# Performance work log

Measured on AMD Instinct MI355X. Metric: run time of the kernel, lower is better.

## Reference

```python
import jax, jax.numpy as jnp
import numpy as np

N_NODES = 50000
N_EDGES = 800000


def _sage_mean(x, src, dst, w, W_self, W_neigh, b, n_nodes):
    # DGL SAGEConv('mean') with edge_weight: messages m_e = w_e * h[src_e],
    # h_neigh[v] = sum_{e->v} m_e / in_degree(v)  (zero if no in-edges),
    # out = h @ W_self + h_neigh @ W_neigh + b
    msg = x[src] * w[:, None]                                   # [E, d]
    s = jax.ops.segment_sum(msg, dst, num_segments=n_nodes)     # [N, d]
    deg = jax.ops.segment_sum(jnp.ones_like(w), dst, num_segments=n_nodes)
    h_neigh = s / jnp.clip(deg, 1.0)[:, None]
    return x @ W_self + h_neigh @ W_neigh + b


def setup_inputs() -> dict:
    key = jax.random.key(0)
    ks = jax.random.split(key, 12)
    d_in, d_h = 64, 256
    inp = {
        'features': jax.random.normal(ks[0], (N_NODES, d_in), dtype=jnp.float32),
        'edge_src': jax.random.randint(ks[1], (N_EDGES,), 0, N_NODES, dtype=jnp.int32),
        'edge_dst': jax.random.randint(ks[2], (N_EDGES,), 0, N_NODES, dtype=jnp.int32),
        'edge_weights': jax.random.uniform(ks[3], (N_EDGES,), dtype=jnp.float32),
        'W1_self': jax.random.normal(ks[4], (d_in, d_h), dtype=jnp.float32) * (1.0 / np.sqrt(d_in)),
        'W1_neigh': jax.random.normal(ks[5], (d_in, d_h), dtype=jnp.float32) * (1.0 / np.sqrt(d_in)),
        'b1': jnp.zeros((d_h,), dtype=jnp.float32),
        'W2_self': jax.random.normal(ks[6], (d_h, 128), dtype=jnp.float32) * (1.0 / np.sqrt(d_h)),
        'W2_neigh': jax.random.normal(ks[7], (d_h, 128), dtype=jnp.float32) * (1.0 / np.sqrt(d_h)),
        'b2': jnp.zeros((128,), dtype=jnp.float32),
        'Wl1': jax.random.normal(ks[8], (128, 64), dtype=jnp.float32) * (1.0 / np.sqrt(128)),
        'bl1': jnp.zeros((64,), dtype=jnp.float32),
        'Wl2': jax.random.normal(ks[9], (64, 32), dtype=jnp.float32) * (1.0 / np.sqrt(64)),
        'bl2': jnp.zeros((32,), dtype=jnp.float32),
        'Wl3': jax.random.normal(ks[10], (32, 10), dtype=jnp.float32) * (1.0 / np.sqrt(32)),
        'bl3': jnp.zeros((10,), dtype=jnp.float32),
    }
    return inp


def reference(features, edge_src, edge_dst, edge_weights,
              W1_self, W1_neigh, b1, W2_self, W2_neigh, b2,
              Wl1, bl1, Wl2, bl2, Wl3, bl3):
    n = features.shape[0]
    x = features.reshape(n, -1)  # flatten (already 2D)
    x = jax.nn.relu(_sage_mean(x, edge_src, edge_dst, edge_weights,
                               W1_self, W1_neigh, b1, n))
    # conv2 is applied twice on identical inputs in the original; results are equal
    embeddings = _sage_mean(x, edge_src, edge_dst, edge_weights,
                            W2_self, W2_neigh, b2, n)
    h = jax.nn.relu(embeddings @ Wl1 + bl1)
    h = jax.nn.relu(h @ Wl2 + bl2)
    out = h @ Wl3 + bl3
    return (out, embeddings)
```

## Files before the change

### kernel.cpp

```cpp
#include <hip/hip_runtime.h>
#include <hip/hip_bf16.h>

#define N_NODES 50000
#define N_EDGES 800000
#define MT_TILES 3125

#define NBLK_SORT 200
#define CHUNK_SORT 4000
#define NBKT 196

typedef __attribute__((ext_vector_type(8))) short frag_ab;
typedef __attribute__((ext_vector_type(4))) float frag_cd;

static __device__ __forceinline__ unsigned short f2b(float f) {
    union { float f; unsigned u; } v; v.f = f;
    unsigned r = v.u + 0x7fffu + ((v.u >> 16) & 1u);
    return (unsigned short)(r >> 16);
}
static __device__ __forceinline__ float b2f(unsigned short b) {
    union { float f; unsigned u; } v; v.u = ((unsigned)b) << 16;
    return v.f;
}
static __device__ __forceinline__ float blo(unsigned p) { return b2f((unsigned short)(p & 0xffffu)); }
static __device__ __forceinline__ float bhi(unsigned p) { return b2f((unsigned short)(p >> 16)); }

static __device__ __forceinline__ unsigned short packBK_elem(const float* __restrict__ Wa,
                                                             const float* __restrict__ Wb,
                                                             int Ka, int N, int idx) {
    int j = idx & 7;
    int lane = (idx >> 3) & 63;
    int rest = idx >> 9;
    int ntiles = N >> 4;
    int nt = rest % ntiles;
    int kt = rest / ntiles;
    int kk = kt * 32 + (lane >> 4) * 8 + j;
    int nn = nt * 16 + (lane & 15);
    float v = (kk < Ka) ? Wa[kk * N + nn] : Wb[(kk - Ka) * N + nn];
    return f2b(v);
}
static __device__ __forceinline__ unsigned short packBN_elem(const float* __restrict__ Wa,
                                                             const float* __restrict__ Wb,
                                                             int Na, int N, int idx) {
    int j = idx & 7;
    int lane = (idx >> 3) & 63;
    int rest = idx >> 9;
    int ntiles = N >> 4;
    int nt = rest % ntiles;
    int kt = rest / ntiles;
    int kk = kt * 32 + (lane >> 4) * 8 + j;
    int nn = nt * 16 + (lane & 15);
    float v = (nn < Na) ? Wa[kk * Na + nn] : Wb[kk * (N - Na) + (nn - Na)];
    return f2b(v);
}

#define PREP_S0 800000
#define PREP_S1 (PREP_S0 + 32768)
#define PREP_S2 (PREP_S1 + 65536)
#define PREP_S3 (PREP_S2 + 8192)
#define PREP_S4 (PREP_S3 + 2048)
#define PREP_BLKS 3549

__global__ __launch_bounds__(256) void prep_p1_kernel(const float4* __restrict__ x4,
                                                      ushort4* __restrict__ xb4,
                                                      const float* __restrict__ W1s,
                                                      const float* __restrict__ W1n,
                                                      const float* __restrict__ W2s,
                                                      const float* __restrict__ W2n,
                                                      const float* __restrict__ Wl1,
                                                      const float* __restrict__ Wl2,
                                                      unsigned short* __restrict__ B1p,
                                                      unsigned short* __restrict__ B2p,
                                                      unsigned short* __restrict__ Bl1p,
                                                      unsigned short* __restrict__ Bl2p,
                                                      const int* __restrict__ dst,
                                                      int* __restrict__ G) {
    __shared__ int h[256];
    int bid = blockIdx.x;
    int t = threadIdx.x;
    if (bid >= PREP_BLKS) {
        int blk = bid - PREP_BLKS;
        h[t] = 0;
        __syncthreads();
        int base = blk * CHUNK_SORT;
        for (int i = t; i < CHUNK_SORT; i += 256)
            atomicAdd(&h[dst[base + i] >> 8], 1);
        __syncthreads();
        G[blk * 256 + t] = h[t];
        return;
    }
    int idx = bid * 256 + t;
    if (idx < PREP_S0) {
        float4 v = x4[idx];
        ushort4 o;
        o.x = f2b(v.x); o.y = f2b(v.y); o.z = f2b(v.z); o.w = f2b(v.w);
        xb4[idx] = o;
    } else if (idx < PREP_S1) {
        int i = idx - PREP_S0;
        B1p[i] = packBK_elem(W1s, W1n, 64, 256, i);
    } else if (idx < PREP_S2) {
        int i = idx - PREP_S1;
        B2p[i] = packBN_elem(W2s, W2n, 128, 256, i);
    } else if (idx < PREP_S3) {
        int i = idx - PREP_S2;
        Bl1p[i] = packBK_elem(Wl1, Wl1, 128, 64, i);
    } else {
        int i = idx - PREP_S3;
        Bl2p[i] = packBK_elem(Wl2, Wl2, 64, 32, i);
    }
}


__global__ __launch_bounds__(256) void p2a_scan(int* __restrict__ G,
                                                int* __restrict__ colsum) {
    __shared__ int sc[256];
    int b = blockIdx.x;
    int t = threadIdx.x;
    int v = (t < NBLK_SORT) ? G[t * 256 + b] : 0;
    sc[t] = v;
    __syncthreads();
    for (int off = 1; off < 256; off <<= 1) {
        int add = (t >= off) ? sc[t - off] : 0;
        __syncthreads();
        sc[t] += add;
        __syncthreads();
    }
    if (t < NBLK_SORT) G[t * 256 + b] = sc[t] - v;
    if (t == 255) colsum[b] = sc[255];
}

__global__ __launch_bounds__(256) void p3_scatter(const int* __restrict__ src,
                                                  const int* __restrict__ dst,
                                                  const float* __restrict__ w,
                                                  const int* __restrict__ G,
                                                  const int* __restrict__ colsum,
                                                  int* __restrict__ bdst,
                                                  int2* __restrict__ bsedge) {
    __shared__ int cur[256];
    __shared__ int sc[256];
    int t = threadIdx.x;
    int v = colsum[t];
    sc[t] = v;
    __syncthreads();
    for (int off = 1; off < 256; off <<= 1) {
        int add = (t >= off) ? sc[t - off] : 0;
        __syncthreads();
        sc[t] += add;
        __syncthreads();
    }
    cur[t] = G[blockIdx.x * 256 + t] + (sc[t] - v);
    __syncthreads();
    int base = blockIdx.x * CHUNK_SORT;
    for (int i = t; i < CHUNK_SORT; i += 256) {
        int e = base + i;
        int d = dst[e];
        int pos = atomicAdd(&cur[d >> 8], 1);
        bdst[pos] = d;
        bsedge[pos] = make_int2(src[e], __float_as_int(w[e]));
    }
}

__global__ __launch_bounds__(256) void p4_sort(const int* __restrict__ colsum,
                                               const int* __restrict__ bdst,
                                               const int2* __restrict__ bsedge,
                                               int* __restrict__ row_off,
                                               float* __restrict__ inv_deg,
                                               int2* __restrict__ sedge) {
    __shared__ int lcnt[256];
    __shared__ int lcur[256];
    __shared__ int sc[256];
    __shared__ int sE0, sE1;
    int t = threadIdx.x;
    int b = blockIdx.x;
    int cv = colsum[t];
    sc[t] = cv;
    __syncthreads();
    for (int off = 1; off < 256; off <<= 1) {
        int add = (t >= off) ? sc[t - off] : 0;
        __syncthreads();
        sc[t] += add;
        __syncthreads();
    }
    if (t == b) { sE0 = sc[t] - cv; sE1 = sc[t]; }
    lcnt[t] = 0;
    __syncthreads();
    int e0 = sE0, e1 = sE1;
    int d0 = b << 8;
    for (int e = e0 + t; e < e1; e += 256)
        atomicAdd(&lcnt[bdst[e] - d0], 1);
    __syncthreads();
    int v = lcnt[t];
    sc[t] = v;
    __syncthreads();
    for (int off = 1; off < 256; off <<= 1) {
        int add = (t >= off) ? sc[t - off] : 0;
        __syncthreads();
        sc[t] += add;
        __syncthreads();
    }
    int loff = e0 + sc[t] - v;
    lcur[t] = loff;
    int d = d0 + t;
    if (d < N_NODES) {
        row_off[d] = loff;
        inv_deg[d] = 1.0f / (float)(v > 0 ? v : 1);
    }
    if (b == 0 && t == 0) row_off[N_NODES] = N_EDGES;
    __syncthreads();
    for (int e = e0 + t; e < e1; e += 256) {
        int dd = bdst[e];
        int2 sv = bsedge[e];
        int pos = atomicAdd(&lcur[dd - d0], 1);
        sedge[pos] = sv;
    }
}


__global__ __launch_bounds__(256) void agg64_kernel(const uint4* __restrict__ xb4,
                                                    const int* __restrict__ row_off,
                                                    const int2* __restrict__ sedge,
                                                    const float* __restrict__ inv_deg,
                                                    uint4* __restrict__ hn1b4) {
    int tid = threadIdx.x;
    int lane = tid & 63;
    int er = lane >> 3;
    int l7 = lane & 7;
    int n = blockIdx.x * 4 + (tid >> 6);
    if (n >= N_NODES) return;
    int e0 = row_off[n], e1 = row_off[n + 1];
    float id = inv_deg[n];
    float a[8];
    #pragma unroll
    for (int j = 0; j < 8; j++) a[j] = 0.f;
    int e1m1 = e1 - 1;
    for (int e = e0; e < e1; e += 16) {
        int2 m[2];
        uint4 p[2];
        float w[2];
        #pragma unroll
        for (int k = 0; k < 2; k++) {
            int ee = e + k * 8 + er;
            int idx = ee < e1 ? ee : e1m1;
            m[k] = sedge[idx];
        }
        #pragma unroll
        for (int k = 0; k < 2; k++) {
            p[k] = xb4[m[k].x * 8 + l7];
            int ee = e + k * 8 + er;
            w[k] = (ee < e1) ? __int_as_float(m[k].y) : 0.f;
        }
        #pragma unroll
        for (int k = 0; k < 2; k++) {
            a[0] += w[k] * blo(p[k].x); a[1] += w[k] * bhi(p[k].x);
            a[2] += w[k] * blo(p[k].y); a[3] += w[k] * bhi(p[k].y);
            a[4] += w[k] * blo(p[k].z); a[5] += w[k] * bhi(p[k].z);
            a[6] += w[k] * blo(p[k].w); a[7] += w[k] * bhi(p[k].w);
        }
    }
    #pragma unroll
    for (int j = 0; j < 8; j++) {
        a[j] += __shfl_xor(a[j], 8, 64);
        a[j] += __shfl_xor(a[j], 16, 64);
        a[j] += __shfl_xor(a[j], 32, 64);
    }
    if (er == 0) {
        uint4 o;
        o.x = (unsigned)f2b(a[0] * id) | ((unsigned)f2b(a[1] * id) << 16);
        o.y = (unsigned)f2b(a[2] * id) | ((unsigned)f2b(a[3] * id) << 16);
        o.z = (unsigned)f2b(a[4] * id) | ((unsigned)f2b(a[5] * id) << 16);
        o.w = (unsigned)f2b(a[6] * id) | ((unsigned)f2b(a[7] * id) << 16);
        hn1b4[n * 8 + l7] = o;
    }
}

__global__ __launch_bounds__(256) void agg128_kernel(const uint4* __restrict__ zb4,
                                                     const int* __restrict__ row_off,
                                                     const int2* __restrict__ sedge,
                                                     const float* __restrict__ inv_deg,
                                                     float* __restrict__ emb,
                                                     uint4* __restrict__ embb4) {
    int tid = threadIdx.x;
    int lane = tid & 63;
    int qr = lane >> 4;
    int l15 = lane & 15;
    int n = blockIdx.x * 4 + (tid >> 6);
    if (n >= N_NODES) return;
    int e0 = row_off[n], e1 = row_off[n + 1];
    float id = inv_deg[n];
    float4 s0, s1;
    if (qr == 0) {
        s0 = ((const float4*)emb)[n * 32 + l15 * 2];
        s1 = ((const float4*)emb)[n * 32 + l15 * 2 + 1];
    }
    float a[8];
    #pragma unroll
    for (int j = 0; j < 8; j++) a[j] = 0.f;
    int e1m1 = e1 - 1;
    for (int e = e0; e < e1; e += 16) {
        int2 m[4];
        uint4 p[4];
        float w[4];
        #pragma unroll
        for (int k = 0; k < 4; k++) {
            int ee = e + k * 4 + qr;
            int idx = ee < e1 ? ee : e1m1;
            m[k] = sedge[idx];
        }
        #pragma unroll
        for (int k = 0; k < 4; k++) {
            p[k] = zb4[m[k].x * 16 + l15];
            int ee = e + k * 4 + qr;
            w[k] = (ee < e1) ? __int_as_float(m[k].y) : 0.f;
        }
        #pragma unroll
        for (int k = 0; k < 4; k++) {
            a[0] += w[k] * blo(p[k].x); a[1] += w[k] * bhi(p[k].x);
            a[2] += w[k] * blo(p[k].y); a[3] += w[k] * bhi(p[k].y);
            a[4] += w[k] * blo(p[k].z); a[5] += w[k] * bhi(p[k].z);
            a[6] += w[k] * blo(p[k].w); a[7] += w[k] * bhi(p[k].w);
        }
    }
    #pragma unroll
    for (int j = 0; j < 8; j++) {
        a[j] += __shfl_xor(a[j], 16, 64);
        a[j] += __shfl_xor(a[j], 32, 64);
    }
    if (qr == 0) {
        float v0 = s0.x + a[0] * id;
        float v1 = s0.y + a[1] * id;
        float v2 = s0.z + a[2] * id;
        float v3 = s0.w + a[3] * id;
        float v4 = s1.x + a[4] * id;
        float v5 = s1.y + a[5] * id;
        float v6 = s1.z + a[6] * id;
        float v7 = s1.w + a[7] * id;
        ((float4*)emb)[n * 32 + l15 * 2]     = make_float4(v0, v1, v2, v3);
        ((float4*)emb)[n * 32 + l15 * 2 + 1] = make_float4(v4, v5, v6, v7);
        uint4 o;
        o.x = (unsigned)f2b(v0) | ((unsigned)f2b(v1) << 16);
        o.y = (unsigned)f2b(v2) | ((unsigned)f2b(v3) << 16);
        o.z = (unsigned)f2b(v4) | ((unsigned)f2b(v5) << 16);
        o.w = (unsigned)f2b(v6) | ((unsigned)f2b(v7) << 16);
        embb4[n * 16 + l15] = o;
    }
}


__global__ __launch_bounds__(512) void gemm1_mfma(const unsigned short* __restrict__ xb,
                                                  const unsigned short* __restrict__ hn1b,
                                                  const unsigned short* __restrict__ Bp,
                                                  const float* __restrict__ b1,
                                                  unsigned short* __restrict__ x1b) {
    __shared__ __align__(16) unsigned short sB[2][8192];
    int tid = threadIdx.x;
    int lane = tid & 63;
    int wv = tid >> 6;
    int mt = blockIdx.x * 8 + wv;
    if (mt >= MT_TILES) mt = MT_TILES - 1;
    int q = lane >> 4;
    int rl = lane & 15;
    int row = mt * 16 + rl;
    frag_ab a[4];
    a[0] = *(const frag_ab*)(xb + row * 64 + q * 8);
    a[1] = *(const frag_ab*)(xb + row * 64 + q * 8 + 32);
    a[2] = *(const frag_ab*)(hn1b + row * 64 + q * 8);
    a[3] = *(const frag_ab*)(hn1b + row * 64 + q * 8 + 32);
    frag_cd acc[16];
    #pragma unroll
    for (int nt = 0; nt < 16; nt++) acc[nt] = (frag_cd){0.f, 0.f, 0.f, 0.f};
    const float4* gB = (const float4*)Bp;
    float4 s0 = gB[tid], s1 = gB[512 + tid];
    ((float4*)sB[0])[tid] = s0;
    ((float4*)sB[0])[512 + tid] = s1;
    #pragma unroll
    for (int kt = 0; kt < 4; kt++) {
        __syncthreads();
        if (kt < 3) { s0 = gB[(kt + 1) * 1024 + tid]; s1 = gB[(kt + 1) * 1024 + 512 + tid]; }
        const unsigned short* sb = sB[kt & 1];
        #pragma unroll
        for (int nt = 0; nt < 16; nt++) {
            frag_ab b = *(const frag_ab*)(sb + (nt * 64 + lane) * 8);
            acc[nt] = __builtin_amdgcn_mfma_f32_16x16x32_bf16(a[kt], b, acc[nt], 0, 0, 0);
        }
        if (kt < 3) {
            ((float4*)sB[(kt + 1) & 1])[tid] = s0;
            ((float4*)sB[(kt + 1) & 1])[512 + tid] = s1;
        }
    }
    int r0 = mt * 16;
    #pragma unroll
    for (int nt = 0; nt < 16; nt++) {
        int c = nt * 16 + rl;
        float bias = b1[c];
        #pragma unroll
        for (int i = 0; i < 4; i++) {
            int r = r0 + q * 4 + i;
            float v = acc[nt][i] + bias;
            v = v > 0.f ? v : 0.f;
            x1b[r * 256 + c] = f2b(v);
        }
    }
}

__global__ __launch_bounds__(512) void gemm2_mfma(const unsigned short* __restrict__ x1b,
                                                  const unsigned short* __restrict__ Bp,
                                                  const float* __restrict__ b2,
                                                  float* __restrict__ emb,
                                                  unsigned short* __restrict__ zb) {
    __shared__ __align__(16) unsigned short sB[2][8192];
    int tid = threadIdx.x;
    int lane = tid & 63;
    int wv = tid >> 6;
    int mt = blockIdx.x * 8 + wv;
    if (mt >= MT_TILES) mt = MT_TILES - 1;
    int q = lane >> 4;
    int rl = lane & 15;
    int row = mt * 16 + rl;
    const unsigned short* arow = x1b + row * 256 + q * 8;
    frag_ab a[8];
    #pragma unroll
    for (int kt = 0; kt < 8; kt++) a[kt] = *(const frag_ab*)(arow + kt * 32);
    frag_cd acc[16];
    #pragma unroll
    for (int nt = 0; nt < 16; nt++) acc[nt] = (frag_cd){0.f, 0.f, 0.f, 0.f};
    const float4* gB = (const float4*)Bp;
    float4 s0 = gB[tid], s1 = gB[512 + tid];
    ((float4*)sB[0])[tid] = s0;
    ((float4*)sB[0])[512 + tid] = s1;
    #pragma unroll
    for (int kt = 0; kt < 8; kt++) {
        __syncthreads();
        if (kt < 7) { s0 = gB[(kt + 1) * 1024 + tid]; s1 = gB[(kt + 1) * 1024 + 512 + tid]; }
        const unsigned short* sb = sB[kt & 1];
        #pragma unroll
        for (int nt = 0; nt < 16; nt++) {
            frag_ab b = *(const frag_ab*)(sb + (nt * 64 + lane) * 8);
            acc[nt] = __builtin_amdgcn_mfma_f32_16x16x32_bf16(a[kt], b, acc[nt], 0, 0, 0);
        }
        if (kt < 7) {
            ((float4*)sB[(kt + 1) & 1])[tid] = s0;
            ((float4*)sB[(kt + 1) & 1])[512 + tid] = s1;
        }
    }
    int r0 = mt * 16;
    #pragma unroll
    for (int nt = 0; nt < 8; nt++) {
        int c = nt * 16 + rl;
        float bias = b2[c];
        #pragma unroll
        for (int i = 0; i < 4; i++) {
            int r = r0 + q * 4 + i;
            emb[r * 128 + c] = acc[nt][i] + bias;
        }
    }
    #pragma unroll
    for (int nt = 8; nt < 16; nt++) {
        int c = (nt - 8) * 16 + rl;
        #pragma unroll
        for (int i = 0; i < 4; i++) {
            int r = r0 + q * 4 + i;
            zb[r * 128 + c] = f2b(acc[nt][i]);
        }
    }
}

__global__ __launch_bounds__(256) void mlp_fused(const unsigned short* __restrict__ embb,
                                                 const unsigned short* __restrict__ B1,
                                                 const float* __restrict__ bl1,
                                                 const unsigned short* __restrict__ B2,
                                                 const float* __restrict__ bl2,
                                                 const float* __restrict__ Wl3,
                                                 const float* __restrict__ bl3,
                                                 float* __restrict__ out) {
    __shared__ __align__(16) unsigned short h64s[64 * 72];
    __shared__ float hs[64][33];
    int tid = threadIdx.x;
    int lane = tid & 63;
    int wv = tid >> 6;
    int mt = blockIdx.x * 4 + wv;
    if (mt >= MT_TILES) mt = MT_TILES - 1;
    int q = lane >> 4;
    int rl = lane & 15;
    const unsigned short* arow = embb + (mt * 16 + rl) * 128 + q * 8;
    const frag_ab* bp1 = (const frag_ab*)B1;
    frag_cd acc[4];
    #pragma unroll
    for (int nt = 0; nt < 4; nt++) acc[nt] = (frag_cd){0.f, 0.f, 0.f, 0.f};
    #pragma unroll
    for (int kt = 0; kt < 4; kt++) {
        frag_ab a = *(const frag_ab*)(arow + kt * 32);
        #pragma unroll
        for (int nt = 0; nt < 4; nt++)
            acc[nt] = __builtin_amdgcn_mfma_f32_16x16x32_bf16(a, bp1[(kt * 4 + nt) * 64 + lane], acc[nt], 0, 0, 0);
    }
    #pragma unroll
    for (int nt = 0; nt < 4; nt++) {
        int c = nt * 16 + rl;
        float bias = bl1[c];
        #pragma unroll
        for (int i = 0; i < 4; i++) {
            float v = acc[nt][i] + bias;
            h64s[(wv * 16 + q * 4 + i) * 72 + c] = f2b(v > 0.f ? v : 0.f);
        }
    }
    __syncthreads();
    const unsigned short* a2 = h64s + (wv * 16 + rl) * 72 + q * 8;
    const frag_ab* bp2 = (const frag_ab*)B2;
    frag_cd acc2[2];
    #pragma unroll
    for (int nt = 0; nt < 2; nt++) acc2[nt] = (frag_cd){0.f, 0.f, 0.f, 0.f};
    #pragma unroll
    for (int kt = 0; kt < 2; kt++) {
        frag_ab a = *(const frag_ab*)(a2 + kt * 32);
        #pragma unroll
        for (int nt = 0; nt < 2; nt++)
            acc2[nt] = __builtin_amdgcn_mfma_f32_16x16x32_bf16(a, bp2[(kt * 2 + nt) * 64 + lane], acc2[nt], 0, 0, 0);
    }
    #pragma unroll
    for (int nt = 0; nt < 2; nt++) {
        int c = nt * 16 + rl;
        float bias = bl2[c];
        #pragma unroll
        for (int i = 0; i < 4; i++) {
            int lr = wv * 16 + q * 4 + i;
            float v = acc2[nt][i] + bias;
            hs[lr][c] = v > 0.f ? v : 0.f;
        }
    }
    __syncthreads();
    int base = blockIdx.x * 64;
    for (int idx = tid; idx < 640; idx += 256) {
        int lr = idx / 10;
        int j = idx - lr * 10;
        int n = base + lr;
        if (n < N_NODES) {
            float a = bl3[j];
            #pragma unroll
            for (int k = 0; k < 32; k++) a += hs[lr][k] * Wl3[k * 10 + j];
            out[n * 10 + j] = a;
        }
    }
}


extern "C" void kernel_launch(void* const* d_in, const int* in_sizes, int n_in,
                              void* d_out, int out_size, void* d_ws, size_t ws_size,
                              hipStream_t stream) {
    const float* x   = (const float*)d_in[0];
    const int* esrc  = (const int*)d_in[1];
    const int* edst  = (const int*)d_in[2];
    const float* ew  = (const float*)d_in[3];
    const float* W1s = (const float*)d_in[4];
    const float* W1n = (const float*)d_in[5];
    const float* b1  = (const float*)d_in[6];
    const float* W2s = (const float*)d_in[7];
    const float* W2n = (const float*)d_in[8];
    const float* b2  = (const float*)d_in[9];
    const float* Wl1 = (const float*)d_in[10];
    const float* bl1 = (const float*)d_in[11];
    const float* Wl2 = (const float*)d_in[12];
    const float* bl2 = (const float*)d_in[13];
    const float* Wl3 = (const float*)d_in[14];
    const float* bl3 = (const float*)d_in[15];

    float* out = (float*)d_out;
    float* emb = out + 500000;

    char* ws = (char*)d_ws;
    size_t off = 0;
    auto alloc = [&](size_t bytes) -> void* {
        void* p = ws + off;
        off = (off + bytes + 255) & ~(size_t)255;
        return p;
    };
    int*   row_off = (int*)alloc((size_t)(N_NODES + 1) * 4);
    float* inv_deg = (float*)alloc((size_t)N_NODES * 4);
    int*   G       = (int*)alloc((size_t)NBLK_SORT * 256 * 4);
    int*   colsum  = (int*)alloc(256 * 4);
    int*   bdst    = (int*)alloc((size_t)N_EDGES * 4);
    int2*  bsedge  = (int2*)alloc((size_t)N_EDGES * 8);
    int2*  sedge   = (int2*)alloc((size_t)N_EDGES * 8);
    unsigned short* xb   = (unsigned short*)alloc((size_t)N_NODES * 64 * 2);
    unsigned short* hn1b = (unsigned short*)alloc((size_t)N_NODES * 64 * 2);
    unsigned short* x1b  = (unsigned short*)alloc((size_t)N_NODES * 256 * 2);
    unsigned short* zb   = (unsigned short*)alloc((size_t)N_NODES * 128 * 2);
    unsigned short* embb = (unsigned short*)alloc((size_t)N_NODES * 128 * 2);
    unsigned short* B1p  = (unsigned short*)alloc(128 * 256 * 2);
    unsigned short* B2p  = (unsigned short*)alloc(256 * 256 * 2);
    unsigned short* Bl1p = (unsigned short*)alloc(128 * 64 * 2);
    unsigned short* Bl2p = (unsigned short*)alloc(64 * 32 * 2);

    prep_p1_kernel<<<PREP_BLKS + NBLK_SORT, 256, 0, stream>>>(
        (const float4*)x, (ushort4*)xb, W1s, W1n, W2s, W2n, Wl1, Wl2,
        B1p, B2p, Bl1p, Bl2p, edst, G);

    p2a_scan<<<256, 256, 0, stream>>>(G, colsum);
    p3_scatter<<<NBLK_SORT, 256, 0, stream>>>(esrc, edst, ew, G, colsum, bdst, bsedge);
    p4_sort<<<NBKT, 256, 0, stream>>>(colsum, bdst, bsedge, row_off, inv_deg, sedge);

    const int GBLK8 = (MT_TILES + 7) / 8;
    const int GBLK  = (MT_TILES + 3) / 4;
    const int ABLK  = (N_NODES + 3) / 4;

    agg64_kernel<<<ABLK, 256, 0, stream>>>((const uint4*)xb, row_off, sedge,
                                           inv_deg, (uint4*)hn1b);
    gemm1_mfma<<<GBLK8, 512, 0, stream>>>(xb, hn1b, B1p, b1, x1b);

    gemm2_mfma<<<GBLK8, 512, 0, stream>>>(x1b, B2p, b2, emb, zb);
    agg128_kernel<<<ABLK, 256, 0, stream>>>((const uint4*)zb, row_off, sedge,
                                            inv_deg, emb, (uint4*)embb);

    mlp_fused<<<GBLK, 256, 0, stream>>>(embb, Bl1p, bl1, Bl2p, bl2, Wl3, bl3, out);
}
```

Before: 234.1 us.

## Fuse layer-1 and layer-2 GEMMs via LDS, drop bf16 embedding copy, widen sort

Merges gemm1 and gemm2 into one kernel that keeps the ReLU'd 256-wide hidden tile in shared memory instead of writing x1b to global memory and reading it back. The agg128 kernel no longer writes a bf16 copy of the embeddings; mlp_fused instead reads fp32 emb and converts it to bf16 in registers. The sort now uses 400 blocks of 2000 edges, and the scan handles two block entries per thread. The fused GEMM drops to 256-thread blocks with a single-buffered B tile and two barriers per k-step, which may lower overlap and occupancy because of the large LDS footprint.

```diff
diff --git a/kernel.cpp b/kernel.cpp
--- a/kernel.cpp
+++ b/kernel.cpp
@@ -5,8 +5,8 @@
 #define N_EDGES 800000
 #define MT_TILES 3125
 
-#define NBLK_SORT 200
-#define CHUNK_SORT 4000
+#define NBLK_SORT 400
+#define CHUNK_SORT 2000
 #define NBKT 196
 
 typedef __attribute__((ext_vector_type(8))) short frag_ab;
@@ -115,7 +115,10 @@
     __shared__ int sc[256];
     int b = blockIdx.x;
     int t = threadIdx.x;
-    int v = (t < NBLK_SORT) ? G[t * 256 + b] : 0;
+    int j0 = 2 * t, j1 = 2 * t + 1;
+    int v0 = (j0 < NBLK_SORT) ? G[j0 * 256 + b] : 0;
+    int v1 = (j1 < NBLK_SORT) ? G[j1 * 256 + b] : 0;
+    int v = v0 + v1;
     sc[t] = v;
     __syncthreads();
     for (int off = 1; off < 256; off <<= 1) {
@@ -124,7 +127,9 @@
         sc[t] += add;
         __syncthreads();
     }
-    if (t < NBLK_SORT) G[t * 256 + b] = sc[t] - v;
+    int ex = sc[t] - v;
+    if (j0 < NBLK_SORT) G[j0 * 256 + b] = ex;
+    if (j1 < NBLK_SORT) G[j1 * 256 + b] = ex + v0;
     if (t == 255) colsum[b] = sc[255];
 }
 
@@ -276,8 +281,7 @@
                                                      const int* __restrict__ row_off,
                                                      const int2* __restrict__ sedge,
                                                      const float* __restrict__ inv_deg,
-                                                     float* __restrict__ emb,
-                                                     uint4* __restrict__ embb4) {
+                                                     float* __restrict__ emb) {
     int tid = threadIdx.x;
     int lane = tid & 63;
     int qr = lane >> 4;
@@ -335,26 +339,23 @@
         float v7 = s1.w + a[7] * id;
         ((float4*)emb)[n * 32 + l15 * 2]     = make_float4(v0, v1, v2, v3);
         ((float4*)emb)[n * 32 + l15 * 2 + 1] = make_float4(v4, v5, v6, v7);
-        uint4 o;
-        o.x = (unsigned)f2b(v0) | ((unsigned)f2b(v1) << 16);
-        o.y = (unsigned)f2b(v2) | ((unsigned)f2b(v3) << 16);
-        o.z = (unsigned)f2b(v4) | ((unsigned)f2b(v5) << 16);
-        o.w = (unsigned)f2b(v6) | ((unsigned)f2b(v7) << 16);
-        embb4[n * 16 + l15] = o;
-    }
-}
-
-
-__global__ __launch_bounds__(512) void gemm1_mfma(const unsigned short* __restrict__ xb,
-                                                  const unsigned short* __restrict__ hn1b,
-                                                  const unsigned short* __restrict__ Bp,
-                                                  const float* __restrict__ b1,
-                                                  unsigned short* __restrict__ x1b) {
-    __shared__ __align__(16) unsigned short sB[2][8192];
+    }
+}
+
+__global__ __launch_bounds__(256) void gemm12_mfma(const unsigned short* __restrict__ xb,
+                                                   const unsigned short* __restrict__ hn1b,
+                                                   const unsigned short* __restrict__ B1p,
+                                                   const float* __restrict__ b1,
+                                                   const unsigned short* __restrict__ B2p,
+                                                   const float* __restrict__ b2,
+                                                   float* __restrict__ emb,
+                                                   unsigned short* __restrict__ zb) {
+    __shared__ __align__(16) unsigned short xS[64 * 264];
+    __shared__ __align__(16) unsigned short sB[8192];
     int tid = threadIdx.x;
     int lane = tid & 63;
     int wv = tid >> 6;
-    int mt = blockIdx.x * 8 + wv;
+    int mt = blockIdx.x * 4 + wv;
     if (mt >= MT_TILES) mt = MT_TILES - 1;
     int q = lane >> 4;
     int rl = lane & 15;
@@ -367,78 +368,60 @@
     frag_cd acc[16];
     #pragma unroll
     for (int nt = 0; nt < 16; nt++) acc[nt] = (frag_cd){0.f, 0.f, 0.f, 0.f};
-    const float4* gB = (const float4*)Bp;
-    float4 s0 = gB[tid], s1 = gB[512 + tid];
-    ((float4*)sB[0])[tid] = s0;
-    ((float4*)sB[0])[512 + tid] = s1;
+    const float4* gB = (const float4*)B1p;
+    float4 s0 = gB[tid], s1 = gB[256 + tid], s2 = gB[512 + tid], s3 = gB[768 + tid];
     #pragma unroll
     for (int kt = 0; kt < 4; kt++) {
         __syncthreads();
-        if (kt < 3) { s0 = gB[(kt + 1) * 1024 + tid]; s1 = gB[(kt + 1) * 1024 + 512 + tid]; }
-        const unsigned short* sb = sB[kt & 1];
+        ((float4*)sB)[tid] = s0;
+        ((float4*)sB)[256 + tid] = s1;
+        ((float4*)sB)[512 + tid] = s2;
+        ((float4*)sB)[768 + tid] = s3;
+        __syncthreads();
+        if (kt < 3) {
+            s0 = gB[(kt + 1) * 1024 + tid];       s1 = gB[(kt + 1) * 1024 + 256 + tid];
+            s2 = gB[(kt + 1) * 1024 + 512 + tid]; s3 = gB[(kt + 1) * 1024 + 768 + tid];
+        }
         #pragma unroll
         for (int nt = 0; nt < 16; nt++) {
-            frag_ab b = *(const frag_ab*)(sb + (nt * 64 + lane) * 8);
+            frag_ab b = *(const frag_ab*)(sB + (nt * 64 + lane) * 8);
             acc[nt] = __builtin_amdgcn_mfma_f32_16x16x32_bf16(a[kt], b, acc[nt], 0, 0, 0);
         }
-        if (kt < 3) {
-            ((float4*)sB[(kt + 1) & 1])[tid] = s0;
-            ((float4*)sB[(kt + 1) & 1])[512 + tid] = s1;
-        }
-    }
-    int r0 = mt * 16;
+    }
     #pragma unroll
     for (int nt = 0; nt < 16; nt++) {
         int c = nt * 16 + rl;
         float bias = b1[c];
         #pragma unroll
         for (int i = 0; i < 4; i++) {
-            int r = r0 + q * 4 + i;
             float v = acc[nt][i] + bias;
             v = v > 0.f ? v : 0.f;
-            x1b[r * 256 + c] = f2b(v);
-        }
-    }
-}
-
-__global__ __launch_bounds__(512) void gemm2_mfma(const unsigned short* __restrict__ x1b,
-                                                  const unsigned short* __restrict__ Bp,
-                                                  const float* __restrict__ b2,
-                                                  float* __restrict__ emb,
-                                                  unsigned short* __restrict__ zb) {
-    __shared__ __align__(16) unsigned short sB[2][8192];
-    int tid = threadIdx.x;
-    int lane = tid & 63;
-    int wv = tid >> 6;
-    int mt = blockIdx.x * 8 + wv;
-    if (mt >= MT_TILES) mt = MT_TILES - 1;
-    int q = lane >> 4;
-    int rl = lane & 15;
-    int row = mt * 16 + rl;
-    const unsigned short* arow = x1b + row * 256 + q * 8;
-    frag_ab a[8];
-    #pragma unroll
-    for (int kt = 0; kt < 8; kt++) a[kt] = *(const frag_ab*)(arow + kt * 32);
-    frag_cd acc[16];
-    #pragma unroll
-    for (int nt = 0; nt < 16; nt++) acc[nt] = (frag_cd){0.f, 0.f, 0.f, 0.f};
-    const float4* gB = (const float4*)Bp;
-    float4 s0 = gB[tid], s1 = gB[512 + tid];
-    ((float4*)sB[0])[tid] = s0;
-    ((float4*)sB[0])[512 + tid] = s1;
+            xS[(wv * 16 + q * 4 + i) * 264 + c] = f2b(v);
+        }
+    }
+    const float4* gB2 = (const float4*)B2p;
+    s0 = gB2[tid]; s1 = gB2[256 + tid]; s2 = gB2[512 + tid]; s3 = gB2[768 + tid];
+    frag_cd acc2[16];
+    #pragma unroll
+    for (int nt = 0; nt < 16; nt++) acc2[nt] = (frag_cd){0.f, 0.f, 0.f, 0.f};
+    const unsigned short* a2base = xS + (wv * 16 + rl) * 264 + q * 8;
     #pragma unroll
     for (int kt = 0; kt < 8; kt++) {
         __syncthreads();
-        if (kt < 7) { s0 = gB[(kt + 1) * 1024 + tid]; s1 = gB[(kt + 1) * 1024 + 512 + tid]; }
-        const unsigned short* sb = sB[kt & 1];
+        ((float4*)sB)[tid] = s0;
+        ((float4*)sB)[256 + tid] = s1;
+        ((float4*)sB)[512 + tid] = s2;
+        ((float4*)sB)[768 + tid] = s3;
+        __syncthreads();
+        if (kt < 7) {
+            s0 = gB2[(kt + 1) * 1024 + tid];       s1 = gB2[(kt + 1) * 1024 + 256 + tid];
+            s2 = gB2[(kt + 1) * 1024 + 512 + tid]; s3 = gB2[(kt + 1) * 1024 + 768 + tid];
+        }
+        frag_ab a2 = *(const frag_ab*)(a2base + kt * 32);
         #pragma unroll
         for (int nt = 0; nt < 16; nt++) {
-            frag_ab b = *(const frag_ab*)(sb + (nt * 64 + lane) * 8);
-            acc[nt] = __builtin_amdgcn_mfma_f32_16x16x32_bf16(a[kt], b, acc[nt], 0, 0, 0);
-        }
-        if (kt < 7) {
-            ((float4*)sB[(kt + 1) & 1])[tid] = s0;
-            ((float4*)sB[(kt + 1) & 1])[512 + tid] = s1;
+            frag_ab b = *(const frag_ab*)(sB + (nt * 64 + lane) * 8);
+            acc2[nt] = __builtin_amdgcn_mfma_f32_16x16x32_bf16(a2, b, acc2[nt], 0, 0, 0);
         }
     }
     int r0 = mt * 16;
@@ -449,7 +432,7 @@
         #pragma unroll
         for (int i = 0; i < 4; i++) {
             int r = r0 + q * 4 + i;
-            emb[r * 128 + c] = acc[nt][i] + bias;
+            emb[r * 128 + c] = acc2[nt][i] + bias;
         }
     }
     #pragma unroll
@@ -458,12 +441,12 @@
         #pragma unroll
         for (int i = 0; i < 4; i++) {
             int r = r0 + q * 4 + i;
-            zb[r * 128 + c] = f2b(acc[nt][i]);
-        }
-    }
-}
-
-__global__ __launch_bounds__(256) void mlp_fused(const unsigned short* __restrict__ embb,
+            zb[r * 128 + c] = f2b(acc2[nt][i]);
+        }
+    }
+}
+
+__global__ __launch_bounds__(256) void mlp_fused(const float* __restrict__ emb,
                                                  const unsigned short* __restrict__ B1,
                                                  const float* __restrict__ bl1,
                                                  const unsigned short* __restrict__ B2,
@@ -480,14 +463,19 @@
     if (mt >= MT_TILES) mt = MT_TILES - 1;
     int q = lane >> 4;
     int rl = lane & 15;
-    const unsigned short* arow = embb + (mt * 16 + rl) * 128 + q * 8;
     const frag_ab* bp1 = (const frag_ab*)B1;
     frag_cd acc[4];
     #pragma unroll
     for (int nt = 0; nt < 4; nt++) acc[nt] = (frag_cd){0.f, 0.f, 0.f, 0.f};
     #pragma unroll
     for (int kt = 0; kt < 4; kt++) {
-        frag_ab a = *(const frag_ab*)(arow + kt * 32);
+        const float4* ap = (const float4*)(emb + (mt * 16 + rl) * 128 + kt * 32 + q * 8);
+        float4 f0 = ap[0], f1 = ap[1];
+        frag_ab a;
+        a[0] = (short)f2b(f0.x); a[1] = (short)f2b(f0.y);
+        a[2] = (short)f2b(f0.z); a[3] = (short)f2b(f0.w);
+        a[4] = (short)f2b(f1.x); a[5] = (short)f2b(f1.y);
+        a[6] = (short)f2b(f1.z); a[7] = (short)f2b(f1.w);
         #pragma unroll
         for (int nt = 0; nt < 4; nt++)
             acc[nt] = __builtin_amdgcn_mfma_f32_16x16x32_bf16(a, bp1[(kt * 4 + nt) * 64 + lane], acc[nt], 0, 0, 0);
@@ -581,9 +569,7 @@
     int2*  sedge   = (int2*)alloc((size_t)N_EDGES * 8);
     unsigned short* xb   = (unsigned short*)alloc((size_t)N_NODES * 64 * 2);
     unsigned short* hn1b = (unsigned short*)alloc((size_t)N_NODES * 64 * 2);
-    unsigned short* x1b  = (unsigned short*)alloc((size_t)N_NODES * 256 * 2);
     unsigned short* zb   = (unsigned short*)alloc((size_t)N_NODES * 128 * 2);
-    unsigned short* embb = (unsigned short*)alloc((size_t)N_NODES * 128 * 2);
     unsigned short* B1p  = (unsigned short*)alloc(128 * 256 * 2);
     unsigned short* B2p  = (unsigned short*)alloc(256 * 256 * 2);
     unsigned short* Bl1p = (unsigned short*)alloc(128 * 64 * 2);
@@ -597,17 +583,15 @@
     p3_scatter<<<NBLK_SORT, 256, 0, stream>>>(esrc, edst, ew, G, colsum, bdst, bsedge);
     p4_sort<<<NBKT, 256, 0, stream>>>(colsum, bdst, bsedge, row_off, inv_deg, sedge);
 
-    const int GBLK8 = (MT_TILES + 7) / 8;
-    const int GBLK  = (MT_TILES + 3) / 4;
-    const int ABLK  = (N_NODES + 3) / 4;
+    const int GBLK = (MT_TILES + 3) / 4;
+    const int ABLK = (N_NODES + 3) / 4;
 
     agg64_kernel<<<ABLK, 256, 0, stream>>>((const uint4*)xb, row_off, sedge,
                                            inv_deg, (uint4*)hn1b);
-    gemm1_mfma<<<GBLK8, 512, 0, stream>>>(xb, hn1b, B1p, b1, x1b);
-
-    gemm2_mfma<<<GBLK8, 512, 0, stream>>>(x1b, B2p, b2, emb, zb);
+    gemm12_mfma<<<GBLK, 256, 0, stream>>>(xb, hn1b, B1p, b1, B2p, b2, emb, zb);
+
     agg128_kernel<<<ABLK, 256, 0, stream>>>((const uint4*)zb, row_off, sedge,
-                                            inv_deg, emb, (uint4*)embb);
-
-    mlp_fused<<<GBLK, 256, 0, stream>>>(embb, Bl1p, bl1, Bl2p, bl2, Wl3, bl3, out);
-}
+                                            inv_deg, emb);
+
+    mlp_fused<<<GBLK, 256, 0, stream>>>(emb, Bl1p, bl1, Bl2p, bl2, Wl3, bl3, out);
+}
```

Result: slower. 241.7 us (+3.2%).

## Drop bf16 embedding copy, convert fp32 embeddings in MLP; double sort blocks

Applied to the files above, without the earlier changes.

agg128 no longer writes a bf16 copy of the embeddings. mlp_fused now reads the fp32 embeddings directly and converts them to bf16 in registers before the MFMA. This saves one 12.8MB write but doubles the read traffic of the MLP input. Separately, the edge-sort partition now uses 400 blocks of 2000 edges instead of 200 of 4000, and the scan handles two block rows per thread.

```diff
diff --git a/kernel.cpp b/kernel.cpp
--- a/kernel.cpp
+++ b/kernel.cpp
@@ -5,8 +5,8 @@
 #define N_EDGES 800000
 #define MT_TILES 3125
 
-#define NBLK_SORT 200
-#define CHUNK_SORT 4000
+#define NBLK_SORT 400
+#define CHUNK_SORT 2000
 #define NBKT 196
 
 typedef __attribute__((ext_vector_type(8))) short frag_ab;
@@ -115,7 +115,10 @@
     __shared__ int sc[256];
     int b = blockIdx.x;
     int t = threadIdx.x;
-    int v = (t < NBLK_SORT) ? G[t * 256 + b] : 0;
+    int j0 = 2 * t, j1 = 2 * t + 1;
+    int v0 = (j0 < NBLK_SORT) ? G[j0 * 256 + b] : 0;
+    int v1 = (j1 < NBLK_SORT) ? G[j1 * 256 + b] : 0;
+    int v = v0 + v1;
     sc[t] = v;
     __syncthreads();
     for (int off = 1; off < 256; off <<= 1) {
@@ -124,7 +127,9 @@
         sc[t] += add;
         __syncthreads();
     }
-    if (t < NBLK_SORT) G[t * 256 + b] = sc[t] - v;
+    int ex = sc[t] - v;
+    if (j0 < NBLK_SORT) G[j0 * 256 + b] = ex;
+    if (j1 < NBLK_SORT) G[j1 * 256 + b] = ex + v0;
     if (t == 255) colsum[b] = sc[255];
 }
 
@@ -276,8 +281,7 @@
                                                      const int* __restrict__ row_off,
                                                      const int2* __restrict__ sedge,
                                                      const float* __restrict__ inv_deg,
-                                                     float* __restrict__ emb,
-                                                     uint4* __restrict__ embb4) {
+                                                     float* __restrict__ emb) {
     int tid = threadIdx.x;
     int lane = tid & 63;
     int qr = lane >> 4;
@@ -335,12 +339,6 @@
         float v7 = s1.w + a[7] * id;
         ((float4*)emb)[n * 32 + l15 * 2]     = make_float4(v0, v1, v2, v3);
         ((float4*)emb)[n * 32 + l15 * 2 + 1] = make_float4(v4, v5, v6, v7);
-        uint4 o;
-        o.x = (unsigned)f2b(v0) | ((unsigned)f2b(v1) << 16);
-        o.y = (unsigned)f2b(v2) | ((unsigned)f2b(v3) << 16);
-        o.z = (unsigned)f2b(v4) | ((unsigned)f2b(v5) << 16);
-        o.w = (unsigned)f2b(v6) | ((unsigned)f2b(v7) << 16);
-        embb4[n * 16 + l15] = o;
     }
 }
 
@@ -463,7 +461,7 @@
     }
 }
 
-__global__ __launch_bounds__(256) void mlp_fused(const unsigned short* __restrict__ embb,
+__global__ __launch_bounds__(256) void mlp_fused(const float* __restrict__ emb,
                                                  const unsigned short* __restrict__ B1,
                                                  const float* __restrict__ bl1,
                                                  const unsigned short* __restrict__ B2,
@@ -480,14 +478,19 @@
     if (mt >= MT_TILES) mt = MT_TILES - 1;
     int q = lane >> 4;
     int rl = lane & 15;
-    const unsigned short* arow = embb + (mt * 16 + rl) * 128 + q * 8;
     const frag_ab* bp1 = (const frag_ab*)B1;
     frag_cd acc[4];
     #pragma unroll
     for (int nt = 0; nt < 4; nt++) acc[nt] = (frag_cd){0.f, 0.f, 0.f, 0.f};
     #pragma unroll
     for (int kt = 0; kt < 4; kt++) {
-        frag_ab a = *(const frag_ab*)(arow + kt * 32);
+        const float4* ap = (const float4*)(emb + (mt * 16 + rl) * 128 + kt * 32 + q * 8);
+        float4 f0 = ap[0], f1 = ap[1];
+        frag_ab a;
+        a[0] = (short)f2b(f0.x); a[1] = (short)f2b(f0.y);
+        a[2] = (short)f2b(f0.z); a[3] = (short)f2b(f0.w);
+        a[4] = (short)f2b(f1.x); a[5] = (short)f2b(f1.y);
+        a[6] = (short)f2b(f1.z); a[7] = (short)f2b(f1.w);
         #pragma unroll
         for (int nt = 0; nt < 4; nt++)
             acc[nt] = __builtin_amdgcn_mfma_f32_16x16x32_bf16(a, bp1[(kt * 4 + nt) * 64 + lane], acc[nt], 0, 0, 0);
@@ -583,7 +586,6 @@
     unsigned short* hn1b = (unsigned short*)alloc((size_t)N_NODES * 64 * 2);
     unsigned short* x1b  = (unsigned short*)alloc((size_t)N_NODES * 256 * 2);
     unsigned short* zb   = (unsigned short*)alloc((size_t)N_NODES * 128 * 2);
-    unsigned short* embb = (unsigned short*)alloc((size_t)N_NODES * 128 * 2);
     unsigned short* B1p  = (unsigned short*)alloc(128 * 256 * 2);
     unsigned short* B2p  = (unsigned short*)alloc(256 * 256 * 2);
     unsigned short* Bl1p = (unsigned short*)alloc(128 * 64 * 2);
@@ -607,7 +609,7 @@
 
     gemm2_mfma<<<GBLK8, 512, 0, stream>>>(x1b, B2p, b2, emb, zb);
     agg128_kernel<<<ABLK, 256, 0, stream>>>((const uint4*)zb, row_off, sedge,
-                                            inv_deg, emb, (uint4*)embb);
-
-    mlp_fused<<<GBLK, 256, 0, stream>>>(embb, Bl1p, bl1, Bl2p, bl2, Wl3, bl3, out);
-}
+                                            inv_deg, emb);
+
+    mlp_fused<<<GBLK, 256, 0, stream>>>(emb, Bl1p, bl1, Bl2p, bl2, Wl3, bl3, out);
+}
```

Measured after the change: 235.0 us. No clear change (+0.4%).
